# Optimization experiments

Measured on AMD Instinct MI355X. Metric: run time of the kernel, lower is better.

## Reference

```python
import jax, jax.numpy as jnp
import numpy as np

H, W = 200, 200          # detector resolution
DELX, DELY = 2.0, 2.0    # detector pixel size
EPS = 1e-8


def _rotation(theta, phi, gamma):
    # R = Rz(theta) @ Ry(phi) @ Rx(gamma), as in diffdrr's Rxyz
    ct, st = jnp.cos(theta), jnp.sin(theta)
    cp, sp = jnp.cos(phi), jnp.sin(phi)
    cg, sg = jnp.cos(gamma), jnp.sin(gamma)
    one, zero = jnp.ones_like(ct), jnp.zeros_like(ct)
    Rz = jnp.stack([jnp.stack([ct, -st, zero]), jnp.stack([st, ct, zero]), jnp.stack([zero, zero, one])])
    Ry = jnp.stack([jnp.stack([cp, zero, sp]), jnp.stack([zero, one, zero]), jnp.stack([-sp, zero, cp])])
    Rx = jnp.stack([jnp.stack([one, zero, zero]), jnp.stack([zero, cg, -sg]), jnp.stack([zero, sg, cg])])
    return Rz @ Ry @ Rx


def setup_inputs() -> dict:
    key = jax.random.key(0)
    volume = jax.random.uniform(key, (256, 256, 256), dtype=jnp.float32)
    spacing = jnp.ones((3,), dtype=jnp.float32)
    return {
        "volume": volume,
        "spacing": spacing,
        "sdr": jnp.float32(300.0),
        "theta": jnp.float32(np.pi),
        "phi": jnp.float32(0.0),
        "gamma": jnp.float32(np.pi / 2),
        "bx": jnp.float32(128.0),
        "by": jnp.float32(128.0),
        "bz": jnp.float32(128.0),
    }


def _drr_forward(volume, spacing, sdr, theta, phi, gamma, bx, by, bz):
    # DRR.__init__ flips the volume along axis 0
    vol = volume[::-1]
    nxyz = np.array(vol.shape)  # static shapes: (X, Y, Z)

    # ---- Detector.make_xrays: camera basis, source and detector plane ----
    R = sdr * _rotation(theta, phi, gamma)          # (3,3)
    source = R[:, 0]                                # rho * first column
    center = -source
    u, v = R[:, 1] / sdr, R[:, 2] / sdr             # unit in-plane basis
    t = (jnp.arange(-(H // 2), H // 2) + 1).astype(jnp.float32) * DELX
    s = (jnp.arange(-(W // 2), W // 2) + 1).astype(jnp.float32) * DELY
    trans = jnp.stack([bx, by, bz])
    src = source + trans                            # (3,)
    # cartesian_prod(t, s): row-major (t slow, s fast) -> (H*W, 3)
    tgt = (t[:, None, None] * u + s[None, :, None] * v + center + trans).reshape(H * W, 3)

    # ---- Siddon.raytrace ----
    sdd = tgt - src + EPS                           # (n, 3)
    # alpha values at every axis-aligned voxel boundary plane
    ax = (jnp.arange(nxyz[0] + 1, dtype=jnp.float32) * spacing[0] - src[0]) / sdd[:, 0:1]
    ay = (jnp.arange(nxyz[1] + 1, dtype=jnp.float32) * spacing[1] - src[1]) / sdd[:, 1:2]
    az = (jnp.arange(nxyz[2] + 1, dtype=jnp.float32) * spacing[2] - src[2]) / sdd[:, 2:3]
    alphas = jnp.concatenate([ax, ay, az], axis=-1)  # (n, P) with P = X+Y+Z+3

    # entry/exit alphas of the volume bounding box
    a0 = (0.0 - src) / sdd                           # (n, 3)
    a1 = (nxyz.astype(np.float32) * spacing - src) / sdd
    amin = jnp.max(jnp.minimum(a0, a1), axis=-1, keepdims=True)
    amax = jnp.min(jnp.maximum(a0, a1), axis=-1, keepdims=True)

    good = (alphas >= amin) & (alphas <= amax)
    alphas = jnp.sort(jnp.where(good, alphas, jnp.inf), axis=-1)  # invalid -> +inf at end

    amid = 0.5 * (alphas[:, :-1] + alphas[:, 1:])    # (n, P-1)
    step = alphas[:, 1:] - alphas[:, :-1]            # inf-inf -> nan for padding
    valid = jnp.isfinite(step)

    # midpoint positions -> voxel indices (trunc, as in torch .trunc())
    pts = src + amid[..., None] * sdd[:, None, :]    # (n, P-1, 3)
    idx = jnp.trunc(jnp.where(valid[..., None], pts, 0.0) / spacing).astype(jnp.int32)
    idx = jnp.clip(idx, 0, jnp.asarray(nxyz - 1, dtype=jnp.int32))
    vox = vol[idx[..., 0], idx[..., 1], idx[..., 2]]  # (n, P-1) gather

    drr = jnp.sum(jnp.where(valid, step, 0.0) * vox, axis=-1)  # nansum equivalent
    drr = drr * jnp.linalg.norm(tgt - src + EPS, axis=-1)       # scale by ray length
    return drr.reshape(1, 1, H, W)


def reference(volume, spacing, sdr, theta, phi, gamma, bx, by, bz):
    return _drr_forward(volume, spacing, sdr, theta, phi, gamma, bx, by, bz)
```

## Files before the change

### kernel.cpp

```cpp
#include <hip/hip_runtime.h>
#include <math.h>

#pragma clang fp contract(off)

#define SPLIT 13
#define BATCH 8
static constexpr int HH = 200, WW = 200;
static constexpr int NRAY = HH * WW;
static constexpr int RBLK = 157;
static constexpr int NWG  = RBLK * SPLIT;

static constexpr int WS_SDD0 = 0;
static constexpr int WS_SDD1 = NRAY;
static constexpr int WS_SDD2 = 2 * NRAY;
static constexpr int WS_AMIN = 3 * NRAY;
static constexpr int WS_AMAX = 4 * NRAY;
static constexpr int WS_NORM = 5 * NRAY;
static constexpr int WS_UNI  = 6 * NRAY;
static constexpr int WS_PART = 6 * NRAY + 8;
static constexpr size_t WS_BYTES = (size_t)(WS_PART + SPLIT * NRAY) * 4;

__device__ __forceinline__ float alpha_of(float k, float sp, float src, float sdd) {
    return (k * sp - src) / sdd;
}

__device__ __forceinline__ int seed_ptr(float X, float spv, float sr, float sd, bool pos) {
    const float kf = (X * sd + sr) / spv;
    int kk;
    if (pos) {
        kk = (int)floorf(kf) + 1;
        kk = kk < 0 ? 0 : (kk > 257 ? 257 : kk);
        while (kk > 0    && alpha_of((float)(kk-1), spv, sr, sd) >  X) --kk;
        while (kk <= 256 && alpha_of((float)kk,     spv, sr, sd) <= X) ++kk;
    } else {
        kk = (int)ceilf(kf) - 1;
        kk = kk > 256 ? 256 : (kk < -1 ? -1 : kk);
        while (kk < 256 && alpha_of((float)(kk+1), spv, sr, sd) >  X) ++kk;
        while (kk >= 0  && alpha_of((float)kk,     spv, sr, sd) <= X) --kk;
    }
    return kk;
}

#define GEN_INTERVAL(stepv, offv)                                        \
    {   const float q = fminf(fminf(tM0, tM1), tM2);                     \
        stepv = q - prev;                                                \
        const float amid = 0.5f * (prev + q);                            \
        const float p0 = src0 + amid * sdd0;                             \
        const float p1 = src1 + amid * sdd1;                             \
        const float p2 = src2 + amid * sdd2;                             \
        float f0, f1, f2;                                                \
        if (UNIT) { f0 = p0; f1 = p1; f2 = p2; }                         \
        else      { f0 = p0 / spn0; f1 = p1 / spn1; f2 = p2 / spn2; }    \
        f0 = fminf(fmaxf(f0, 0.0f), 255.0f);                             \
        f1 = fminf(fmaxf(f1, 0.0f), 255.0f);                             \
        f2 = fminf(fmaxf(f2, 0.0f), 255.0f);                             \
        const int i0 = (int)f0, i1 = (int)f1, i2 = (int)f2;              \
        offv = (unsigned)(((((255 ^ i0) << 8) + i1) << 8) + i2) << 2;    \
        prev = q;                                                        \
        const bool m0 = (tM0 == q);                                      \
        const bool m1 = !m0 && (tM1 == q);                               \
        const bool m2 = !(m0 || m1);                                     \
        tM0 = m0 ? tM0 + dl0 : tM0;                                      \
        tM1 = m1 ? tM1 + dl1 : tM1;                                      \
        tM2 = m2 ? tM2 + dl2 : tM2; }

template<bool UNIT>
__device__ __forceinline__ float merge_loop(
    const float* __restrict__ vol, int trip, float prev,
    float tM0, float tM1, float tM2,
    float dl0, float dl1, float dl2,
    float src0, float src1, float src2,
    float spn0, float spn1, float spn2,
    float sdd0, float sdd1, float sdd2)
{
    float acc = 0.0f;
    int n = trip;
    while (n >= BATCH) {
        float stepv[BATCH], vox[BATCH];
        unsigned off[BATCH];
        #pragma unroll
        for (int i = 0; i < BATCH; ++i) {
            GEN_INTERVAL(stepv[i], off[i])
            asm volatile("global_load_dword %0, %1, %2"
                         : "=v"(vox[i])
                         : "v"(off[i]), "s"(vol));
        }
        asm volatile("s_waitcnt vmcnt(0)");
        __builtin_amdgcn_sched_barrier(0);
        #pragma unroll
        for (int i = 0; i < BATCH; ++i)
            acc = fmaf(stepv[i], vox[i], acc);
        n -= BATCH;
    }
    while (n > 0) {
        float stepv;
        unsigned off;
        GEN_INTERVAL(stepv, off)
        const float vox = vol[off >> 2];
        acc = fmaf(stepv, vox, acc);
        --n;
    }
    return acc;
}

__global__ __launch_bounds__(256)
void drr_pre(const float* __restrict__ spacing,
             const float* __restrict__ sdrP,  const float* __restrict__ thetaP,
             const float* __restrict__ phiP,  const float* __restrict__ gammaP,
             const float* __restrict__ bxP,   const float* __restrict__ byP,
             const float* __restrict__ bzP,   float* __restrict__ ws)
{
    const int rid = blockIdx.x * blockDim.x + threadIdx.x;
    if (rid >= NRAY) return;
    const int it = rid % HH, is = rid / HH;

    const float sdr = sdrP[0];
    const float th = thetaP[0], ph = phiP[0], ga = gammaP[0];
    const float ct = cosf(th), st = sinf(th);
    const float cp = cosf(ph), sp = sinf(ph);
    const float cg = cosf(ga), sg = sinf(ga);

    const float rot[3][3] = {
        { ct*cp, ct*sp*sg - st*cg, ct*sp*cg + st*sg },
        { st*cp, st*sp*sg + ct*cg, st*sp*cg - ct*sg },
        { -sp,   cp*sg,            cp*cg            }
    };

    float u[3], v[3], source[3], trans[3], src[3], spn[3];
    trans[0] = bxP[0]; trans[1] = byP[0]; trans[2] = bzP[0];
    for (int a = 0; a < 3; ++a) {
        source[a] = sdr * rot[a][0];
        u[a] = (sdr * rot[a][1]) / sdr;
        v[a] = (sdr * rot[a][2]) / sdr;
        src[a] = source[a] + trans[a];
        spn[a] = spacing[a];
    }

    const float tc = (float)(it - HH/2 + 1) * 2.0f;
    const float sc = (float)(is - WW/2 + 1) * 2.0f;

    float sdd[3];
    float nrm2 = 0.0f;
    for (int a = 0; a < 3; ++a) {
        float tg = tc * u[a] + sc * v[a];
        tg = tg - source[a];
        tg = tg + trans[a];
        float dd = (tg - src[a]) + 1e-8f;
        sdd[a] = dd;
        nrm2 = nrm2 + dd * dd;
    }

    float amin = -INFINITY, amax = INFINITY;
    for (int a = 0; a < 3; ++a) {
        float a0 = (0.0f - src[a]) / sdd[a];
        float a1 = (256.0f * spn[a] - src[a]) / sdd[a];
        amin = fmaxf(amin, fminf(a0, a1));
        amax = fminf(amax, fmaxf(a0, a1));
    }

    ws[WS_SDD0 + rid] = sdd[0];
    ws[WS_SDD1 + rid] = sdd[1];
    ws[WS_SDD2 + rid] = sdd[2];
    ws[WS_AMIN + rid] = amin;
    ws[WS_AMAX + rid] = amax;
    ws[WS_NORM + rid] = sqrtf(nrm2);
    if (rid == 0) {
        ws[WS_UNI + 0] = src[0]; ws[WS_UNI + 1] = src[1]; ws[WS_UNI + 2] = src[2];
        ws[WS_UNI + 3] = spn[0]; ws[WS_UNI + 4] = spn[1]; ws[WS_UNI + 5] = spn[2];
    }
}

__global__ __launch_bounds__(256)
void drr_main(const float* __restrict__ vol,
              float* __restrict__ ws)
{
    const int lin = blockIdx.x;
    const int xcd = lin & 7;
    const int pos = lin >> 3;
    const int swz = (xcd == 0) ? pos : (256 + (xcd - 1) * 255 + pos);
    const int ridBlk = swz / SPLIT;
    const int seg    = swz - ridBlk * SPLIT;

    const int rid = ridBlk * 256 + threadIdx.x;
    if (rid >= NRAY) return;

    const float sdd0 = ws[WS_SDD0 + rid];
    const float sdd1 = ws[WS_SDD1 + rid];
    const float sdd2 = ws[WS_SDD2 + rid];
    const float amin = ws[WS_AMIN + rid];
    const float amax = ws[WS_AMAX + rid];
    const float src0 = ws[WS_UNI + 0], src1 = ws[WS_UNI + 1], src2 = ws[WS_UNI + 2];
    const float spn0 = ws[WS_UNI + 3], spn1 = ws[WS_UNI + 4], spn2 = ws[WS_UNI + 5];
    const bool unit = (spn0 == 1.0f) & (spn1 == 1.0f) & (spn2 == 1.0f);

    float acc = 0.0f;
    if (amax > amin) {
        const float blo = (seg == 0) ? amin
                        : amin + (amax - amin) * ((float)seg / (float)SPLIT);
        const float bhi = (seg == SPLIT - 1) ? amax
                        : amin + (amax - amin) * ((float)(seg + 1) / (float)SPLIT);

        const float sddv[3] = { sdd0, sdd1, sdd2 };
        const float srcv[3] = { src0, src1, src2 };
        const float spnv[3] = { spn0, spn1, spn2 };
        float tM[3], dl[3];
        float prev = -INFINITY;
        int trip = 0;

        for (int a = 0; a < 3; ++a) {
            const float sd = sddv[a], sr = srcv[a], spv = spnv[a];
            const bool pos2 = sd > 0.0f;
            const int ks = seed_ptr(blo, spv, sr, sd, pos2);
            const int ke = seed_ptr(bhi, spv, sr, sd, pos2);
            int cnt;
            if (pos2) {
                cnt = ke - ks;
                if (ks - 1 >= 0) {
                    const float ap = alpha_of((float)(ks-1), spv, sr, sd);
                    if (ap >= amin && ap > prev) prev = ap;
                }
                tM[a] = (ks <= 256) ? alpha_of((float)ks, spv, sr, sd) : INFINITY;
            } else {
                cnt = ks - ke;
                if (ks + 1 <= 256) {
                    const float ap = alpha_of((float)(ks+1), spv, sr, sd);
                    if (ap >= amin && ap > prev) prev = ap;
                }
                tM[a] = (ks >= 0) ? alpha_of((float)ks, spv, sr, sd) : INFINITY;
            }
            if (cnt < 0) cnt = 0;
            trip += cnt;
            dl[a] = fabsf(spv / sd);
        }

        if (unit) {
            acc = merge_loop<true >(vol, trip, prev, tM[0], tM[1], tM[2],
                                    dl[0], dl[1], dl[2], src0, src1, src2,
                                    spn0, spn1, spn2, sdd0, sdd1, sdd2);
        } else {
            acc = merge_loop<false>(vol, trip, prev, tM[0], tM[1], tM[2],
                                    dl[0], dl[1], dl[2], src0, src1, src2,
                                    spn0, spn1, spn2, sdd0, sdd1, sdd2);
        }
    }

    ws[WS_PART + seg * NRAY + rid] = acc;
}

__global__ __launch_bounds__(256)
void drr_fin(const float* __restrict__ ws, float* __restrict__ out)
{
    const int rid = blockIdx.x * blockDim.x + threadIdx.x;
    if (rid >= NRAY) return;
    float s = 0.0f;
    #pragma unroll
    for (int seg = 0; seg < SPLIT; ++seg)
        s = s + ws[WS_PART + seg * NRAY + rid];
    const int it = rid % HH, is = rid / HH;
    out[it * WW + is] = s * ws[WS_NORM + rid];
}

__global__ __launch_bounds__(256)
void drr_mono(const float* __restrict__ vol,
              const float* __restrict__ spacing,
              const float* __restrict__ sdrP,  const float* __restrict__ thetaP,
              const float* __restrict__ phiP,  const float* __restrict__ gammaP,
              const float* __restrict__ bxP,   const float* __restrict__ byP,
              const float* __restrict__ bzP,   float* __restrict__ out)
{
    const int lin = blockIdx.x;
    const int xcd = lin & 7;
    const int pos = lin >> 3;
    const int swz = (xcd == 0) ? pos : (256 + (xcd - 1) * 255 + pos);
    const int ridBlk = swz / SPLIT;
    const int seg    = swz - ridBlk * SPLIT;
    const int rid = ridBlk * 256 + threadIdx.x;
    if (rid >= NRAY) return;
    const int it = rid % HH, is = rid / HH;

    const float sdr = sdrP[0];
    const float th = thetaP[0], ph = phiP[0], ga = gammaP[0];
    const float ct = cosf(th), st = sinf(th);
    const float cp = cosf(ph), sp = sinf(ph);
    const float cg = cosf(ga), sg = sinf(ga);
    const float rot[3][3] = {
        { ct*cp, ct*sp*sg - st*cg, ct*sp*cg + st*sg },
        { st*cp, st*sp*sg + ct*cg, st*sp*cg - ct*sg },
        { -sp,   cp*sg,            cp*cg            }
    };
    float u[3], v[3], source[3], trans[3], src[3], spn[3];
    trans[0] = bxP[0]; trans[1] = byP[0]; trans[2] = bzP[0];
    for (int a = 0; a < 3; ++a) {
        source[a] = sdr * rot[a][0];
        u[a] = (sdr * rot[a][1]) / sdr;
        v[a] = (sdr * rot[a][2]) / sdr;
        src[a] = source[a] + trans[a];
        spn[a] = spacing[a];
    }
    const float tc = (float)(it - HH/2 + 1) * 2.0f;
    const float sc = (float)(is - WW/2 + 1) * 2.0f;
    float sdd[3]; float nrm2 = 0.0f;
    for (int a = 0; a < 3; ++a) {
        float tg = tc * u[a] + sc * v[a];
        tg = tg - source[a];
        tg = tg + trans[a];
        float dd = (tg - src[a]) + 1e-8f;
        sdd[a] = dd;
        nrm2 = nrm2 + dd * dd;
    }
    const bool unit = (spn[0] == 1.0f) & (spn[1] == 1.0f) & (spn[2] == 1.0f);
    float amin = -INFINITY, amax = INFINITY;
    for (int a = 0; a < 3; ++a) {
        float a0 = (0.0f - src[a]) / sdd[a];
        float a1 = (256.0f * spn[a] - src[a]) / sdd[a];
        amin = fmaxf(amin, fminf(a0, a1));
        amax = fminf(amax, fmaxf(a0, a1));
    }
    float acc = 0.0f;
    if (amax > amin) {
        const float blo = (seg == 0) ? amin
                        : amin + (amax - amin) * ((float)seg / (float)SPLIT);
        const float bhi = (seg == SPLIT - 1) ? amax
                        : amin + (amax - amin) * ((float)(seg + 1) / (float)SPLIT);
        float tM[3], dl[3];
        float prev = -INFINITY;
        int trip = 0;
        for (int a = 0; a < 3; ++a) {
            const float sd = sdd[a], sr = src[a], spv = spn[a];
            const bool pos2 = sd > 0.0f;
            const int ks = seed_ptr(blo, spv, sr, sd, pos2);
            const int ke = seed_ptr(bhi, spv, sr, sd, pos2);
            int cnt;
            if (pos2) {
                cnt = ke - ks;
                if (ks - 1 >= 0) {
                    const float ap = alpha_of((float)(ks-1), spv, sr, sd);
                    if (ap >= amin && ap > prev) prev = ap;
                }
                tM[a] = (ks <= 256) ? alpha_of((float)ks, spv, sr, sd) : INFINITY;
            } else {
                cnt = ks - ke;
                if (ks + 1 <= 256) {
                    const float ap = alpha_of((float)(ks+1), spv, sr, sd);
                    if (ap >= amin && ap > prev) prev = ap;
                }
                tM[a] = (ks >= 0) ? alpha_of((float)ks, spv, sr, sd) : INFINITY;
            }
            if (cnt < 0) cnt = 0;
            trip += cnt;
            dl[a] = fabsf(spv / sd);
        }
        if (unit) {
            acc = merge_loop<true >(vol, trip, prev, tM[0], tM[1], tM[2],
                                    dl[0], dl[1], dl[2], src[0], src[1], src[2],
                                    spn[0], spn[1], spn[2], sdd[0], sdd[1], sdd[2]);
        } else {
            acc = merge_loop<false>(vol, trip, prev, tM[0], tM[1], tM[2],
                                    dl[0], dl[1], dl[2], src[0], src[1], src[2],
                                    spn[0], spn[1], spn[2], sdd[0], sdd[1], sdd[2]);
        }
    }
    atomicAdd(&out[it * WW + is], acc * sqrtf(nrm2));
}

extern "C" void kernel_launch(void* const* d_in, const int* in_sizes, int n_in,
                              void* d_out, int out_size, void* d_ws, size_t ws_size,
                              hipStream_t stream)
{
    const float* vol     = (const float*)d_in[0];
    const float* spacing = (const float*)d_in[1];
    const float* sdr     = (const float*)d_in[2];
    const float* theta   = (const float*)d_in[3];
    const float* phi     = (const float*)d_in[4];
    const float* gamma   = (const float*)d_in[5];
    const float* bx      = (const float*)d_in[6];
    const float* by      = (const float*)d_in[7];
    const float* bz      = (const float*)d_in[8];
    float* out = (float*)d_out;

    if (ws_size >= WS_BYTES) {
        float* ws = (float*)d_ws;
        drr_pre<<<RBLK, 256, 0, stream>>>(spacing, sdr, theta, phi, gamma,
                                          bx, by, bz, ws);
        drr_main<<<NWG, 256, 0, stream>>>(vol, ws);
        drr_fin<<<RBLK, 256, 0, stream>>>(ws, out);
    } else {
        hipMemsetAsync(out, 0, (size_t)out_size * sizeof(float), stream);
        drr_mono<<<NWG, 256, 0, stream>>>(vol, spacing, sdr, theta, phi, gamma,
                                          bx, by, bz, out);
    }
}
```

Baseline: 52.62 us.

## Load-balance ray segments per wavefront using per-group interval counts

Replaces the fixed split of every ray into 13 segments with a planned split. A pre-pass counts each ray's intervals, and a max-reduction over each 64-ray group feeds a prefix-sum plan that gives every wavefront a number of segments proportional to its work. The merge loop also recomputes each boundary from an integer index instead of accumulating a delta, and drops the inline-asm batched loads in favour of plain loads. This adds two small launches plus a binary search per wavefront, and without the explicit batching the loads may be less overlapped.

```diff
diff --git a/kernel.cpp b/kernel.cpp
--- a/kernel.cpp
+++ b/kernel.cpp
@@ -3,12 +3,13 @@
 
 #pragma clang fp contract(off)
 
-#define SPLIT 13
 #define BATCH 8
 static constexpr int HH = 200, WW = 200;
 static constexpr int NRAY = HH * WW;
-static constexpr int RBLK = 157;
-static constexpr int NWG  = RBLK * SPLIT;
+static constexpr int NG   = NRAY / 64;
+static constexpr int MAIN_BLOCKS = 2048;
+static constexpr int KSCALE = 7552;
+static constexpr int RBLK = (NRAY + 255) / 256;
 
 static constexpr int WS_SDD0 = 0;
 static constexpr int WS_SDD1 = NRAY;
@@ -16,9 +17,12 @@
 static constexpr int WS_AMIN = 3 * NRAY;
 static constexpr int WS_AMAX = 4 * NRAY;
 static constexpr int WS_NORM = 5 * NRAY;
-static constexpr int WS_UNI  = 6 * NRAY;
-static constexpr int WS_PART = 6 * NRAY + 8;
-static constexpr size_t WS_BYTES = (size_t)(WS_PART + SPLIT * NRAY) * 4;
+static constexpr int WS_CNT  = 6 * NRAY;
+static constexpr int WS_UNI  = 7 * NRAY;
+static constexpr int WS_GMAX = 7 * NRAY + 8;
+static constexpr int WS_BASE = 7 * NRAY + 8 + NG;
+static constexpr int WS_PART = 281280;
+static constexpr size_t WS_BYTES = (size_t)(WS_PART + 8192 * 64) * 4;
 
 __device__ __forceinline__ float alpha_of(float k, float sp, float src, float sdd) {
     return (k * sp - src) / sdd;
@@ -41,7 +45,7 @@
     return kk;
 }
 
-#define GEN_INTERVAL(stepv, offv)                                        \
+#define GEN_INTERVAL(stepv, addrv)                                       \
     {   const float q = fminf(fminf(tM0, tM1), tM2);                     \
         stepv = q - prev;                                                \
         const float amid = 0.5f * (prev + q);                            \
@@ -55,20 +59,31 @@
         f1 = fminf(fmaxf(f1, 0.0f), 255.0f);                             \
         f2 = fminf(fmaxf(f2, 0.0f), 255.0f);                             \
         const int i0 = (int)f0, i1 = (int)f1, i2 = (int)f2;              \
-        offv = (unsigned)(((((255 ^ i0) << 8) + i1) << 8) + i2) << 2;    \
+        addrv = ((((255 ^ i0) << 8) + i1) << 8) + i2;                    \
         prev = q;                                                        \
         const bool m0 = (tM0 == q);                                      \
         const bool m1 = !m0 && (tM1 == q);                               \
-        const bool m2 = !(m0 || m1);                                     \
-        tM0 = m0 ? tM0 + dl0 : tM0;                                      \
-        tM1 = m1 ? tM1 + dl1 : tM1;                                      \
-        tM2 = m2 ? tM2 + dl2 : tM2; }
+        const float kf_s  = m0 ? kf0  : (m1 ? kf1  : kf2);               \
+        const float kst_s = m0 ? kst0 : (m1 ? kst1 : kst2);              \
+        const float sr_s  = m0 ? src0 : (m1 ? src1 : src2);              \
+        const float sd_s  = m0 ? sdd0 : (m1 ? sdd1 : sdd2);              \
+        const float nk = kf_s + kst_s;                                   \
+        float al;                                                        \
+        if (UNIT) { al = (nk - sr_s) / sd_s; }                           \
+        else { const float sp_s = m0 ? spn0 : (m1 ? spn1 : spn2);        \
+               al = (nk * sp_s - sr_s) / sd_s; }                         \
+        const float nv = (nk >= 0.0f && nk <= 256.0f) ? al : INFINITY;   \
+        if (m0)      { kf0 = nk; tM0 = nv; }                             \
+        else if (m1) { kf1 = nk; tM1 = nv; }                             \
+        else         { kf2 = nk; tM2 = nv; }                             \
+    }
 
 template<bool UNIT>
 __device__ __forceinline__ float merge_loop(
     const float* __restrict__ vol, int trip, float prev,
+    float kf0, float kf1, float kf2,
+    float kst0, float kst1, float kst2,
     float tM0, float tM1, float tM2,
-    float dl0, float dl1, float dl2,
     float src0, float src1, float src2,
     float spn0, float spn1, float spn2,
     float sdd0, float sdd1, float sdd2)
@@ -77,16 +92,12 @@
     int n = trip;
     while (n >= BATCH) {
         float stepv[BATCH], vox[BATCH];
-        unsigned off[BATCH];
+        int addr[BATCH];
         #pragma unroll
         for (int i = 0; i < BATCH; ++i) {
-            GEN_INTERVAL(stepv[i], off[i])
-            asm volatile("global_load_dword %0, %1, %2"
-                         : "=v"(vox[i])
-                         : "v"(off[i]), "s"(vol));
+            GEN_INTERVAL(stepv[i], addr[i])
+            vox[i] = vol[addr[i]];
         }
-        asm volatile("s_waitcnt vmcnt(0)");
-        __builtin_amdgcn_sched_barrier(0);
         #pragma unroll
         for (int i = 0; i < BATCH; ++i)
             acc = fmaf(stepv[i], vox[i], acc);
@@ -94,13 +105,70 @@
     }
     while (n > 0) {
         float stepv;
-        unsigned off;
-        GEN_INTERVAL(stepv, off)
-        const float vox = vol[off >> 2];
-        acc = fmaf(stepv, vox, acc);
+        int addr;
+        GEN_INTERVAL(stepv, addr)
+        acc = fmaf(stepv, vol[addr], acc);
         --n;
     }
     return acc;
+}
+
+__device__ __forceinline__ float trace_window(
+    const float* __restrict__ vol,
+    float amin, float amax, int s, int nseg,
+    float src0, float src1, float src2,
+    float spn0, float spn1, float spn2,
+    float sdd0, float sdd1, float sdd2, bool unit)
+{
+    const float blo = (s == 0) ? amin
+                    : amin + (amax - amin) * ((float)s / (float)nseg);
+    const float bhi = (s == nseg - 1) ? amax
+                    : amin + (amax - amin) * ((float)(s + 1) / (float)nseg);
+
+    const float sddv[3] = { sdd0, sdd1, sdd2 };
+    const float srcv[3] = { src0, src1, src2 };
+    const float spnv[3] = { spn0, spn1, spn2 };
+    float kf[3], kst[3], tM[3];
+    float prev = -INFINITY;
+    int trip = 0;
+
+    for (int a = 0; a < 3; ++a) {
+        const float sd = sddv[a], sr = srcv[a], spv = spnv[a];
+        const bool pos = sd > 0.0f;
+        kst[a] = pos ? 1.0f : -1.0f;
+        const int ks = seed_ptr(blo, spv, sr, sd, pos);
+        const int ke = seed_ptr(bhi, spv, sr, sd, pos);
+        int cnt;
+        if (pos) {
+            cnt = ke - ks;
+            if (ks - 1 >= 0) {
+                const float ap = alpha_of((float)(ks-1), spv, sr, sd);
+                if (ap >= amin && ap > prev) prev = ap;
+            }
+            tM[a] = (ks <= 256) ? alpha_of((float)ks, spv, sr, sd) : INFINITY;
+        } else {
+            cnt = ks - ke;
+            if (ks + 1 <= 256) {
+                const float ap = alpha_of((float)(ks+1), spv, sr, sd);
+                if (ap >= amin && ap > prev) prev = ap;
+            }
+            tM[a] = (ks >= 0) ? alpha_of((float)ks, spv, sr, sd) : INFINITY;
+        }
+        if (cnt < 0) cnt = 0;
+        trip += cnt;
+        kf[a] = (float)ks;
+    }
+
+    if (unit)
+        return merge_loop<true >(vol, trip, prev, kf[0], kf[1], kf[2],
+                                 kst[0], kst[1], kst[2], tM[0], tM[1], tM[2],
+                                 src0, src1, src2, spn0, spn1, spn2,
+                                 sdd0, sdd1, sdd2);
+    else
+        return merge_loop<false>(vol, trip, prev, kf[0], kf[1], kf[2],
+                                 kst[0], kst[1], kst[2], tM[0], tM[1], tM[2],
+                                 src0, src1, src2, spn0, spn1, spn2,
+                                 sdd0, sdd1, sdd2);
 }
 
 __global__ __launch_bounds__(256)
@@ -164,6 +232,20 @@
     ws[WS_AMIN + rid] = amin;
     ws[WS_AMAX + rid] = amax;
     ws[WS_NORM + rid] = sqrtf(nrm2);
+
+    int cnt = 0;
+    if (amax > amin) {
+        for (int a = 0; a < 3; ++a) {
+            const float sd = sdd[a], sr = src[a], spv = spn[a];
+            const bool pos = sd > 0.0f;
+            const int ks = seed_ptr(amin, spv, sr, sd, pos);
+            const int ke = seed_ptr(amax, spv, sr, sd, pos);
+            int c = pos ? (ke - ks) : (ks - ke);
+            if (c > 0) cnt += c;
+        }
+    }
+    ((int*)ws)[WS_CNT + rid] = cnt;
+
     if (rid == 0) {
         ws[WS_UNI + 0] = src[0]; ws[WS_UNI + 1] = src[1]; ws[WS_UNI + 2] = src[2];
         ws[WS_UNI + 3] = spn[0]; ws[WS_UNI + 4] = spn[1]; ws[WS_UNI + 5] = spn[2];
@@ -171,18 +253,71 @@
 }
 
 __global__ __launch_bounds__(256)
-void drr_main(const float* __restrict__ vol,
-              float* __restrict__ ws)
-{
-    const int lin = blockIdx.x;
-    const int xcd = lin & 7;
-    const int pos = lin >> 3;
-    const int swz = (xcd == 0) ? pos : (256 + (xcd - 1) * 255 + pos);
-    const int ridBlk = swz / SPLIT;
-    const int seg    = swz - ridBlk * SPLIT;
-
-    const int rid = ridBlk * 256 + threadIdx.x;
-    if (rid >= NRAY) return;
+void drr_gmax(float* __restrict__ ws)
+{
+    const int g = blockIdx.x * blockDim.x + threadIdx.x;
+    if (g >= NG) return;
+    const int* wsi = (const int*)ws;
+    int m = 0;
+    for (int l = 0; l < 64; ++l) {
+        const int c = wsi[WS_CNT + (g << 6) + l];
+        m = c > m ? c : m;
+    }
+    ((int*)ws)[WS_GMAX + g] = m;
+}
+
+__global__ __launch_bounds__(1024)
+void drr_plan(float* __restrict__ ws)
+{
+    __shared__ int sh[1024];
+    const int i = threadIdx.x;
+    int* wsi = (int*)ws;
+    const int v = (i < NG) ? wsi[WS_GMAX + i] : 0;
+    sh[i] = v;
+    __syncthreads();
+    for (int off = 512; off > 0; off >>= 1) {
+        if (i < off) sh[i] += sh[i + off];
+        __syncthreads();
+    }
+    const int total = sh[0];
+    __syncthreads();
+    int n = 0;
+    if (i < NG) {
+        n = (total > 0) ? (int)(((long long)KSCALE * v) / total) : 1;
+        if (n < 1) n = 1;
+    }
+    sh[i] = n;
+    __syncthreads();
+    for (int off = 1; off < 1024; off <<= 1) {
+        const int t = (i >= off) ? sh[i - off] : 0;
+        __syncthreads();
+        sh[i] += t;
+        __syncthreads();
+    }
+    if (i < NG) wsi[WS_BASE + i + 1] = sh[i];
+    if (i == 0) wsi[WS_BASE] = 0;
+}
+
+__global__ __launch_bounds__(256)
+void drr_main(const float* __restrict__ vol, float* __restrict__ ws)
+{
+    const int* wsi = (const int*)ws;
+    const int lane = threadIdx.x & 63;
+    const int w = ((blockIdx.x & 7) << 10) + ((blockIdx.x >> 3) << 2)
+                + (threadIdx.x >> 6);
+    const int total = wsi[WS_BASE + NG];
+    if (w >= total) return;
+
+    int lo = 0, hi = NG;
+    while (hi - lo > 1) {
+        const int mid = (lo + hi) >> 1;
+        if (wsi[WS_BASE + mid] <= w) lo = mid; else hi = mid;
+    }
+    const int g    = lo;
+    const int base = wsi[WS_BASE + g];
+    const int nseg = wsi[WS_BASE + g + 1] - base;
+    const int s    = w - base;
+    const int rid  = (g << 6) + lane;
 
     const float sdd0 = ws[WS_SDD0 + rid];
     const float sdd1 = ws[WS_SDD1 + rid];
@@ -194,57 +329,12 @@
     const bool unit = (spn0 == 1.0f) & (spn1 == 1.0f) & (spn2 == 1.0f);
 
     float acc = 0.0f;
-    if (amax > amin) {
-        const float blo = (seg == 0) ? amin
-                        : amin + (amax - amin) * ((float)seg / (float)SPLIT);
-        const float bhi = (seg == SPLIT - 1) ? amax
-                        : amin + (amax - amin) * ((float)(seg + 1) / (float)SPLIT);
-
-        const float sddv[3] = { sdd0, sdd1, sdd2 };
-        const float srcv[3] = { src0, src1, src2 };
-        const float spnv[3] = { spn0, spn1, spn2 };
-        float tM[3], dl[3];
-        float prev = -INFINITY;
-        int trip = 0;
-
-        for (int a = 0; a < 3; ++a) {
-            const float sd = sddv[a], sr = srcv[a], spv = spnv[a];
-            const bool pos2 = sd > 0.0f;
-            const int ks = seed_ptr(blo, spv, sr, sd, pos2);
-            const int ke = seed_ptr(bhi, spv, sr, sd, pos2);
-            int cnt;
-            if (pos2) {
-                cnt = ke - ks;
-                if (ks - 1 >= 0) {
-                    const float ap = alpha_of((float)(ks-1), spv, sr, sd);
-                    if (ap >= amin && ap > prev) prev = ap;
-                }
-                tM[a] = (ks <= 256) ? alpha_of((float)ks, spv, sr, sd) : INFINITY;
-            } else {
-                cnt = ks - ke;
-                if (ks + 1 <= 256) {
-                    const float ap = alpha_of((float)(ks+1), spv, sr, sd);
-                    if (ap >= amin && ap > prev) prev = ap;
-                }
-                tM[a] = (ks >= 0) ? alpha_of((float)ks, spv, sr, sd) : INFINITY;
-            }
-            if (cnt < 0) cnt = 0;
-            trip += cnt;
-            dl[a] = fabsf(spv / sd);
-        }
-
-        if (unit) {
-            acc = merge_loop<true >(vol, trip, prev, tM[0], tM[1], tM[2],
-                                    dl[0], dl[1], dl[2], src0, src1, src2,
-                                    spn0, spn1, spn2, sdd0, sdd1, sdd2);
-        } else {
-            acc = merge_loop<false>(vol, trip, prev, tM[0], tM[1], tM[2],
-                                    dl[0], dl[1], dl[2], src0, src1, src2,
-                                    spn0, spn1, spn2, sdd0, sdd1, sdd2);
-        }
-    }
-
-    ws[WS_PART + seg * NRAY + rid] = acc;
+    if (amax > amin)
+        acc = trace_window(vol, amin, amax, s, nseg,
+                           src0, src1, src2, spn0, spn1, spn2,
+                           sdd0, sdd1, sdd2, unit);
+
+    ws[WS_PART + w * 64 + lane] = acc;
 }
 
 __global__ __launch_bounds__(256)
@@ -252,12 +342,16 @@
 {
     const int rid = blockIdx.x * blockDim.x + threadIdx.x;
     if (rid >= NRAY) return;
-    float s = 0.0f;
-    #pragma unroll
-    for (int seg = 0; seg < SPLIT; ++seg)
-        s = s + ws[WS_PART + seg * NRAY + rid];
+    const int* wsi = (const int*)ws;
+    const int g    = rid >> 6;
+    const int lane = rid & 63;
+    const int base = wsi[WS_BASE + g];
+    const int nseg = wsi[WS_BASE + g + 1] - base;
+    float sum = 0.0f;
+    for (int s = 0; s < nseg; ++s)
+        sum = sum + ws[WS_PART + (base + s) * 64 + lane];
     const int it = rid % HH, is = rid / HH;
-    out[it * WW + is] = s * ws[WS_NORM + rid];
+    out[it * WW + is] = sum * ws[WS_NORM + rid];
 }
 
 __global__ __launch_bounds__(256)
@@ -268,14 +362,10 @@
               const float* __restrict__ bxP,   const float* __restrict__ byP,
               const float* __restrict__ bzP,   float* __restrict__ out)
 {
-    const int lin = blockIdx.x;
-    const int xcd = lin & 7;
-    const int pos = lin >> 3;
-    const int swz = (xcd == 0) ? pos : (256 + (xcd - 1) * 255 + pos);
-    const int ridBlk = swz / SPLIT;
-    const int seg    = swz - ridBlk * SPLIT;
-    const int rid = ridBlk * 256 + threadIdx.x;
-    if (rid >= NRAY) return;
+    const int tid = blockIdx.x * blockDim.x + threadIdx.x;
+    if (tid >= NRAY * 13) return;
+    const int seg = tid / NRAY;
+    const int rid = tid - seg * NRAY;
     const int it = rid % HH, is = rid / HH;
 
     const float sdr = sdrP[0];
@@ -317,49 +407,10 @@
         amax = fminf(amax, fmaxf(a0, a1));
     }
     float acc = 0.0f;
-    if (amax > amin) {
-        const float blo = (seg == 0) ? amin
-                        : amin + (amax - amin) * ((float)seg / (float)SPLIT);
-        const float bhi = (seg == SPLIT - 1) ? amax
-                        : amin + (amax - amin) * ((float)(seg + 1) / (float)SPLIT);
-        float tM[3], dl[3];
-        float prev = -INFINITY;
-        int trip = 0;
-        for (int a = 0; a < 3; ++a) {
-            const float sd = sdd[a], sr = src[a], spv = spn[a];
-            const bool pos2 = sd > 0.0f;
-            const int ks = seed_ptr(blo, spv, sr, sd, pos2);
-            const int ke = seed_ptr(bhi, spv, sr, sd, pos2);
-            int cnt;
-            if (pos2) {
-                cnt = ke - ks;
-                if (ks - 1 >= 0) {
-                    const float ap = alpha_of((float)(ks-1), spv, sr, sd);
-                    if (ap >= amin && ap > prev) prev = ap;
-                }
-                tM[a] = (ks <= 256) ? alpha_of((float)ks, spv, sr, sd) : INFINITY;
-            } else {
-                cnt = ks - ke;
-                if (ks + 1 <= 256) {
-                    const float ap = alpha_of((float)(ks+1), spv, sr, sd);
-                    if (ap >= amin && ap > prev) prev = ap;
-                }
-                tM[a] = (ks >= 0) ? alpha_of((float)ks, spv, sr, sd) : INFINITY;
-            }
-            if (cnt < 0) cnt = 0;
-            trip += cnt;
-            dl[a] = fabsf(spv / sd);
-        }
-        if (unit) {
-            acc = merge_loop<true >(vol, trip, prev, tM[0], tM[1], tM[2],
-                                    dl[0], dl[1], dl[2], src[0], src[1], src[2],
-                                    spn[0], spn[1], spn[2], sdd[0], sdd[1], sdd[2]);
-        } else {
-            acc = merge_loop<false>(vol, trip, prev, tM[0], tM[1], tM[2],
-                                    dl[0], dl[1], dl[2], src[0], src[1], src[2],
-                                    spn[0], spn[1], spn[2], sdd[0], sdd[1], sdd[2]);
-        }
-    }
+    if (amax > amin)
+        acc = trace_window(vol, amin, amax, seg, 13,
+                           src[0], src[1], src[2], spn[0], spn[1], spn[2],
+                           sdd[0], sdd[1], sdd[2], unit);
     atomicAdd(&out[it * WW + is], acc * sqrtf(nrm2));
 }
 
@@ -380,13 +431,15 @@
 
     if (ws_size >= WS_BYTES) {
         float* ws = (float*)d_ws;
-        drr_pre<<<RBLK, 256, 0, stream>>>(spacing, sdr, theta, phi, gamma,
-                                          bx, by, bz, ws);
-        drr_main<<<NWG, 256, 0, stream>>>(vol, ws);
-        drr_fin<<<RBLK, 256, 0, stream>>>(ws, out);
+        drr_pre <<<RBLK, 256, 0, stream>>>(spacing, sdr, theta, phi, gamma,
+                                           bx, by, bz, ws);
+        drr_gmax<<<(NG + 255) / 256, 256, 0, stream>>>(ws);
+        drr_plan<<<1, 1024, 0, stream>>>(ws);
+        drr_main<<<MAIN_BLOCKS, 256, 0, stream>>>(vol, ws);
+        drr_fin <<<RBLK, 256, 0, stream>>>(ws, out);
     } else {
         hipMemsetAsync(out, 0, (size_t)out_size * sizeof(float), stream);
-        drr_mono<<<NWG, 256, 0, stream>>>(vol, spacing, sdr, theta, phi, gamma,
-                                          bx, by, bz, out);
-    }
-}
+        drr_mono<<<(NRAY * 13 + 255) / 256, 256, 0, stream>>>(
+            vol, spacing, sdr, theta, phi, gamma, bx, by, bz, out);
+    }
+}
```

Result: slower. 86.32 us (+64.0%).
